# Kernel tuning notes

Measured on AMD Instinct MI355X. Metric: run time of the kernel, lower is better.

The kernel has to match this reference:

```python
import jax, jax.numpy as jnp
import numpy as np

B_SZ, L, D_MODEL = 2, 2048, 1024
EXPAND, N_STATE, K = 2, 16, 4
D_INNER = D_MODEL * EXPAND


def setup_inputs() -> dict:
    key = jax.random.key(0)
    ks = jax.random.split(key, 12)
    s = lambda k, shape, scale=0.02: jax.random.normal(k, shape, jnp.float32) * scale
    return {
        "x": jax.random.normal(ks[0], (B_SZ, L, D_MODEL), jnp.float32),
        "ln_gamma": jnp.ones((D_MODEL,), jnp.float32),
        "ln_beta": jnp.zeros((D_MODEL,), jnp.float32),
        "W_in": s(ks[1], (D_MODEL, 2 * D_INNER)),
        "conv_w": s(ks[2], (D_INNER, 1, K), 0.1),
        "conv_b": jnp.zeros((D_INNER,), jnp.float32),
        "A_log": jax.random.normal(ks[3], (N_STATE,), jnp.float32),
        "B_mat": s(ks[4], (N_STATE, D_INNER), 0.05),
        "C_mat": s(ks[5], (D_INNER, N_STATE), 0.05),
        "D_vec": s(ks[6], (D_INNER,), 0.1),
        "Wd": s(ks[7], (D_INNER, D_INNER)),
        "bd": jnp.zeros((D_INNER,), jnp.float32),
        "W_out": s(ks[8], (D_INNER, D_MODEL)),
    }


def _layernorm(x, g, b, eps=1e-5):
    mu = jnp.mean(x, axis=-1, keepdims=True)
    var = jnp.var(x, axis=-1, keepdims=True)
    return (x - mu) * jax.lax.rsqrt(var + eps) * g + b


def _selective_scan(x, delta, A, B_mat, C_mat, D_vec):
    # x: (b,l,d), delta: (b,l), A: (n,)
    dA = jnp.exp(delta[..., None] * A)            # (b,l,n)
    Bx = jnp.einsum('bld,nd->bln', x, B_mat) * delta[..., None]  # (b,l,n)

    def step(h, inp):
        dA_t, Bx_t = inp
        h = dA_t * h + Bx_t
        return h, h

    h0 = jnp.zeros((x.shape[0], A.shape[0]), x.dtype)
    # scan over seq axis
    _, hs = jax.lax.scan(step, h0, (jnp.swapaxes(dA, 0, 1), jnp.swapaxes(Bx, 0, 1)))
    hs = jnp.swapaxes(hs, 0, 1)                   # (b,l,n)
    return jnp.einsum('bln,dn->bld', hs, C_mat) + D_vec * x


def reference(x, ln_gamma, ln_beta, W_in, conv_w, conv_b, A_log, B_mat, C_mat, D_vec, Wd, bd, W_out):
    residual = x
    h = _layernorm(x, ln_gamma, ln_beta)
    xg = h @ W_in                                  # (b,l,2*d_inner)
    xs, gate = jnp.split(xg, 2, axis=-1)
    # depthwise causal conv (torch pads K-1 both sides then slices [:L] == left pad K-1)
    xc = jnp.swapaxes(xs, 1, 2)                    # (b,d,l)
    xc = jax.lax.conv_general_dilated(
        xc, conv_w, window_strides=(1,), padding=((K - 1, 0),),
        dimension_numbers=('NCH', 'OIH', 'NCH'), feature_group_count=D_INNER)
    xc = xc + conv_b[None, :, None]
    xs = jnp.swapaxes(xc, 1, 2)                    # (b,l,d)
    xs = jax.nn.silu(xs)
    # S4 kernel
    delta = jnp.mean(jax.nn.softplus(xs @ Wd + bd), axis=-1)  # (b,l)
    A = -jnp.exp(A_log)
    y = _selective_scan(xs, delta, A, B_mat, C_mat, D_vec)
    y = y * jax.nn.silu(gate)
    y = y @ W_out
    return residual + y
```

## Files before the change

kernel.cpp:

```cpp
#include <hip/hip_runtime.h>
#include <cstdint>
#include <cstddef>

typedef unsigned short u16;
typedef __attribute__((ext_vector_type(4))) float floatx4;
typedef __attribute__((ext_vector_type(8))) __bf16 bf16x8;

__device__ __forceinline__ float u2f(u16 u) {
    union { unsigned int i; float f; } x;
    x.i = ((unsigned int)u) << 16;
    return x.f;
}
__device__ __forceinline__ u16 f2u(float f) {
    union { float f; unsigned int i; } x;
    x.f = f;
    unsigned int r = x.i + 0x7fffu + ((x.i >> 16) & 1u);
    return (u16)(r >> 16);
}

__device__ __forceinline__ void swz(int bid, int& x, int& y) {
    int xcd = bid & 7;
    int lid = bid >> 3;
    x = lid >> 2;
    y = xcd * 4 + (lid & 3);
}

__device__ __forceinline__ void tr_tile(const float* __restrict__ in, u16* __restrict__ out,
                                        int K, int N, int bx, int by, float* tile ) {
    int n0 = bx * 32, k0 = by * 32;
    int tx = threadIdx.x & 31, ty = threadIdx.x >> 5;
#pragma unroll
    for (int j = 0; j < 4; ++j) {
        int r = ty + j * 8;
        tile[r * 33 + tx] = in[(size_t)(k0 + r) * N + n0 + tx];
    }
    __syncthreads();
#pragma unroll
    for (int j = 0; j < 4; ++j) {
        int r = ty + j * 8;
        out[(size_t)(n0 + r) * K + k0 + tx] = f2u(tile[tx * 33 + r]);
    }
}

__global__ __launch_bounds__(256)
void prep_kernel(const float* __restrict__ W_in, u16* __restrict__ Wt_in,
                 const float* __restrict__ Wd, u16* __restrict__ Wt_ext,
                 const float* __restrict__ W_out, u16* __restrict__ Wt_out,
                 const float* __restrict__ B_mat,
                 const float* __restrict__ x, const float* __restrict__ gamma,
                 const float* __restrict__ beta, u16* __restrict__ h,
                 float* __restrict__ out) {
    __shared__ float tile[32 * 33];
    int blk = blockIdx.x, t = threadIdx.x;
    if (blk < 4096) {
        tr_tile(W_in, Wt_in, 1024, 4096, blk & 127, blk >> 7, tile);
    } else if (blk < 8192) {
        int b2 = blk - 4096;
        tr_tile(Wd, Wt_ext, 2048, 2048, b2 & 63, b2 >> 6, tile);
    } else if (blk < 10240) {
        int b3 = blk - 8192;
        tr_tile(W_out, Wt_out, 2048, 1024, b3 & 31, b3 >> 5, tile);
    } else if (blk < 14336) {
        int r = blk - 10240;
        const float4* xr = (const float4*)(x + (size_t)r * 1024);
        float4 xv = xr[t];
        ((float4*)(out + (size_t)r * 1024))[t] = xv;
        float s = xv.x + xv.y + xv.z + xv.w;
        float ss = xv.x * xv.x + xv.y * xv.y + xv.z * xv.z + xv.w * xv.w;
#pragma unroll
        for (int off = 32; off > 0; off >>= 1) {
            s += __shfl_down(s, off, 64);
            ss += __shfl_down(ss, off, 64);
        }
        __shared__ float rs[4], rss[4], mu_s, ri_s;
        int wave = t >> 6, lane = t & 63;
        if (lane == 0) { rs[wave] = s; rss[wave] = ss; }
        __syncthreads();
        if (t == 0) {
            float S = rs[0] + rs[1] + rs[2] + rs[3];
            float SS = rss[0] + rss[1] + rss[2] + rss[3];
            float mu = S * (1.f / 1024.f);
            float var = SS * (1.f / 1024.f) - mu * mu;
            mu_s = mu;
            ri_s = rsqrtf(fmaxf(var, 0.f) + 1e-5f);
        }
        __syncthreads();
        float mu = mu_s, ri = ri_s;
        float4 gv = ((const float4*)gamma)[t];
        float4 bv = ((const float4*)beta)[t];
        ushort4 o;
        o.x = f2u((xv.x - mu) * ri * gv.x + bv.x);
        o.y = f2u((xv.y - mu) * ri * gv.y + bv.y);
        o.z = f2u((xv.z - mu) * ri * gv.z + bv.z);
        o.w = f2u((xv.w - mu) * ri * gv.w + bv.w);
        ((ushort4*)(h + (size_t)r * 1024))[t] = o;
    } else {
        int idx = (blk - 14336) * 256 + t;
        int row = 2048 + (idx >> 11), col = idx & 2047;
        u16 v = (row < 2064) ? f2u(B_mat[(size_t)(row - 2048) * 2048 + col]) : (u16)0;
        Wt_ext[(size_t)row * 2048 + col] = v;
    }
}

__device__ __forceinline__ void gl_lds16(const u16* g, u16* l) {
    __builtin_amdgcn_global_load_lds(
        (const __attribute__((address_space(1))) void*)g,
        (__attribute__((address_space(3))) void*)l, 16, 0, 0);
}

template <int EPI>
__device__ __forceinline__
void gemm128_body(const u16* __restrict__ A, const u16* __restrict__ Bt,
                  void* __restrict__ out, int M, int N, int K, int Ksub) {
    __shared__ u16 As[128 * 64];
    __shared__ u16 Bs[128 * 64];
    int bx, by;
    swz(blockIdx.x, bx, by);
    const int tid = threadIdx.x;
    const int wave = tid >> 6, lane = tid & 63;
    const int row0 = by * 128, col0 = bx * 128;
    const int koff = blockIdx.y * Ksub;
    const int l16 = lane & 15, q = lane >> 4;
    const int sRow = lane >> 2, sK = (lane & 3) * 8;

    floatx4 acc[4][4];
#pragma unroll
    for (int i = 0; i < 4; ++i)
#pragma unroll
        for (int j = 0; j < 4; ++j) acc[i][j] = (floatx4){0.f, 0.f, 0.f, 0.f};

    const u16* gA = A + (size_t)(row0 + wave * 32 + sRow) * K + koff + sK;
    const u16* gB = Bt + (size_t)(col0 + wave * 32 + sRow) * K + koff + sK;
    u16* lA = As + wave * 1024;
    u16* lB = Bs + wave * 1024;
    const int rowb = (wave >> 1) * 64, colb = (wave & 1) * 64;

    for (int k0 = 0; k0 < Ksub; k0 += 64) {
#pragma unroll
        for (int h = 0; h < 2; ++h) {
            gl_lds16(gA + h * 32, lA + h * 4096);
            gl_lds16(gA + (size_t)16 * K + h * 32, lA + h * 4096 + 512);
            gl_lds16(gB + h * 32, lB + h * 4096);
            gl_lds16(gB + (size_t)16 * K + h * 32, lB + h * 4096 + 512);
        }
        gA += 64; gB += 64;
        __syncthreads();
#pragma unroll
        for (int h = 0; h < 2; ++h) {
            bf16x8 af[4], bfr[4];
#pragma unroll
            for (int mi = 0; mi < 4; ++mi)
                af[mi] = *(const bf16x8*)(As + h * 4096 + (rowb + mi * 16 + l16) * 32 + q * 8);
#pragma unroll
            for (int ni = 0; ni < 4; ++ni)
                bfr[ni] = *(const bf16x8*)(Bs + h * 4096 + (colb + ni * 16 + l16) * 32 + q * 8);
#pragma unroll
            for (int mi = 0; mi < 4; ++mi)
#pragma unroll
                for (int ni = 0; ni < 4; ++ni)
                    acc[mi][ni] = __builtin_amdgcn_mfma_f32_16x16x32_bf16(
                        af[mi], bfr[ni], acc[mi][ni], 0, 0, 0);
        }
        __syncthreads();
    }

    const int mB = row0 + rowb;
    const int nB = col0 + colb + l16;
    if constexpr (EPI == 0) {
        u16* o = (u16*)out;
#pragma unroll
        for (int mi = 0; mi < 4; ++mi)
#pragma unroll
            for (int ni = 0; ni < 4; ++ni)
#pragma unroll
                for (int rr = 0; rr < 4; ++rr)
                    o[(size_t)(mB + mi * 16 + q * 4 + rr) * N + nB + ni * 16] =
                        f2u(acc[mi][ni][rr]);
    } else {
        float* C = (float*)out;
#pragma unroll
        for (int mi = 0; mi < 4; ++mi)
#pragma unroll
            for (int ni = 0; ni < 4; ++ni)
#pragma unroll
                for (int rr = 0; rr < 4; ++rr)
                    atomicAdd(&C[(size_t)(mB + mi * 16 + q * 4 + rr) * N + nB + ni * 16],
                              acc[mi][ni][rr]);
    }
}

__global__ __launch_bounds__(256)
void gemm_xg(const u16* __restrict__ A, const u16* __restrict__ Bt,
             u16* __restrict__ out, int M, int N, int K) {
    gemm128_body<0>(A, Bt, out, M, N, K, K);
}

__global__ __launch_bounds__(256)
void gemm_fin(const u16* __restrict__ A, const u16* __restrict__ Bt,
              void* __restrict__ out, int M, int N, int K, int Ksub) {
    gemm128_body<4>(A, Bt, out, M, N, K, Ksub);
}

__global__ __launch_bounds__(256)
void gemm_delta(const u16* __restrict__ A, const u16* __restrict__ Bt,
                float* __restrict__ dacc, const float* __restrict__ bias,
                float* __restrict__ Bdotn, int M, int N, int K) {
    __shared__ u16 As[128 * 128];
    __shared__ u16 Bs[64 * 128];
    int bx, by;
    swz(blockIdx.x, bx, by);
    const int tid = threadIdx.x;
    const int wave = tid >> 6, lane = tid & 63;
    const int row0 = by * 128, col0 = bx * 64;
    const int l16 = lane & 15, q = lane >> 4;
    const int sRow = lane >> 2, sK = (lane & 3) * 8;

    floatx4 acc[2][4];
#pragma unroll
    for (int i = 0; i < 2; ++i)
#pragma unroll
        for (int j = 0; j < 4; ++j) acc[i][j] = (floatx4){0.f, 0.f, 0.f, 0.f};

    const u16* gA = A + (size_t)(row0 + wave * 32 + sRow) * K + sK;
    const u16* gB = Bt + (size_t)(col0 + wave * 16 + sRow) * K + sK;
    u16* lA = As + wave * 1024;
    u16* lB = Bs + wave * 512;
    const int rowb = wave * 32;

    for (int k0 = 0; k0 < K; k0 += 128) {
#pragma unroll
        for (int h = 0; h < 4; ++h) {
            gl_lds16(gA + h * 32, lA + h * 4096);
            gl_lds16(gA + (size_t)16 * K + h * 32, lA + h * 4096 + 512);
            gl_lds16(gB + h * 32, lB + h * 2048);
        }
        gA += 128; gB += 128;
        __syncthreads();
#pragma unroll
        for (int h = 0; h < 4; ++h) {
            bf16x8 af[2], bfr[4];
#pragma unroll
            for (int mi = 0; mi < 2; ++mi)
                af[mi] = *(const bf16x8*)(As + h * 4096 + (rowb + mi * 16 + l16) * 32 + q * 8);
#pragma unroll
            for (int ni = 0; ni < 4; ++ni)
                bfr[ni] = *(const bf16x8*)(Bs + h * 2048 + (ni * 16 + l16) * 32 + q * 8);
#pragma unroll
            for (int mi = 0; mi < 2; ++mi)
#pragma unroll
                for (int ni = 0; ni < 4; ++ni)
                    acc[mi][ni] = __builtin_amdgcn_mfma_f32_16x16x32_bf16(
                        af[mi], bfr[ni], acc[mi][ni], 0, 0, 0);
        }
        __syncthreads();
    }

    const int mB = row0 + rowb;
    const int nB = col0 + l16;
    if (col0 < 2048) {
#pragma unroll
        for (int mi = 0; mi < 2; ++mi) {
#pragma unroll
            for (int rr = 0; rr < 4; ++rr) {
                float sv = 0.f;
#pragma unroll
                for (int ni = 0; ni < 4; ++ni) {
                    float t2 = acc[mi][ni][rr] + bias[nB + ni * 16];
                    sv += (t2 > 20.f) ? t2 : log1pf(expf(t2));
                }
#pragma unroll
                for (int off = 1; off < 16; off <<= 1)
                    sv += __shfl_xor(sv, off, 64);
                if (l16 == 0)
                    atomicAdd(&dacc[mB + mi * 16 + q * 4 + rr], sv);
            }
        }
    } else {
#pragma unroll
        for (int mi = 0; mi < 2; ++mi)
#pragma unroll
            for (int rr = 0; rr < 4; ++rr)
                Bdotn[(size_t)l16 * 4096 + mB + mi * 16 + q * 4 + rr] =
                    acc[mi][0][rr];
    }
}

__global__ __launch_bounds__(256) void conv_silu_kernel(const u16* __restrict__ xg,
                                                        const float* __restrict__ conv_w,
                                                        const float* __restrict__ conv_b,
                                                        u16* __restrict__ xsc,
                                                        float* __restrict__ delta_acc) {
    int r0 = blockIdx.x * 8;
    int l0 = r0 & 2047, bb = r0 >> 11;
    int t = threadIdx.x, d8 = t * 8;
    if (t < 8) delta_acc[r0 + t] = 0.f;

    ushort4 rw[11][2];
#pragma unroll
    for (int j = 0; j < 11; ++j) {
        int ls = l0 + j - 3;
        if (ls >= 0) {
            const u16* row = xg + (size_t)((bb << 11) + ls) * 4096 + d8;
            rw[j][0] = *(const ushort4*)row;
            rw[j][1] = *(const ushort4*)(row + 4);
        } else {
            rw[j][0] = (ushort4){0, 0, 0, 0};
            rw[j][1] = (ushort4){0, 0, 0, 0};
        }
    }
    float w[8][4];
#pragma unroll
    for (int j = 0; j < 8; ++j) {
        float4 wv = *(const float4*)(conv_w + (size_t)(d8 + j) * 4);
        w[j][0] = wv.x; w[j][1] = wv.y; w[j][2] = wv.z; w[j][3] = wv.w;
    }
    float cb[8];
    {
        float4 b0 = *(const float4*)(conv_b + d8);
        float4 b1 = *(const float4*)(conv_b + d8 + 4);
        cb[0] = b0.x; cb[1] = b0.y; cb[2] = b0.z; cb[3] = b0.w;
        cb[4] = b1.x; cb[5] = b1.y; cb[6] = b1.z; cb[7] = b1.w;
    }
#pragma unroll
    for (int i = 0; i < 8; ++i) {
        float xs[8];
#pragma unroll
        for (int j = 0; j < 8; ++j) xs[j] = cb[j];
#pragma unroll
        for (int k = 0; k < 4; ++k) {
            ushort4 u0 = rw[i + k][0], u1 = rw[i + k][1];
            xs[0] += w[0][k] * u2f(u0.x); xs[1] += w[1][k] * u2f(u0.y);
            xs[2] += w[2][k] * u2f(u0.z); xs[3] += w[3][k] * u2f(u0.w);
            xs[4] += w[4][k] * u2f(u1.x); xs[5] += w[5][k] * u2f(u1.y);
            xs[6] += w[6][k] * u2f(u1.z); xs[7] += w[7][k] * u2f(u1.w);
        }
        ushort4 o0, o1;
        o0.x = f2u(xs[0] / (1.f + expf(-xs[0])));
        o0.y = f2u(xs[1] / (1.f + expf(-xs[1])));
        o0.z = f2u(xs[2] / (1.f + expf(-xs[2])));
        o0.w = f2u(xs[3] / (1.f + expf(-xs[3])));
        o1.x = f2u(xs[4] / (1.f + expf(-xs[4])));
        o1.y = f2u(xs[5] / (1.f + expf(-xs[5])));
        o1.z = f2u(xs[6] / (1.f + expf(-xs[6])));
        o1.w = f2u(xs[7] / (1.f + expf(-xs[7])));
        u16* orow = xsc + (size_t)(r0 + i) * 2048 + d8;
        *(ushort4*)orow = o0;
        *(ushort4*)(orow + 4) = o1;
    }
}

__global__ __launch_bounds__(256) void scan_kernel(const float* __restrict__ delta_acc,
                                                   const float* __restrict__ Bdotn,
                                                   const float* __restrict__ A_log,
                                                   float* __restrict__ hsn) {
    int chain = blockIdx.x;
    int b = chain >> 4, n = chain & 15;
    int t = threadIdx.x;
    int wave = t >> 6, lane = t & 63;
    __shared__ float sd[2048], sb[2048];
    __shared__ float wA[4], wB[4];
#pragma unroll
    for (int m = 0; m < 2; ++m) {
        int idx = (m * 256 + t) * 4;
        *(float4*)(sd + idx) = *(const float4*)(delta_acc + b * 2048 + idx);
        *(float4*)(sb + idx) = *(const float4*)(Bdotn + (size_t)n * 4096 + b * 2048 + idx);
    }
    __syncthreads();
    float An = -expf(A_log[n]);
    int base = t * 8;
    float a[8], bb[8];
#pragma unroll
    for (int i = 0; i < 8; ++i) {
        float dl = sd[base + i] * (1.f / 2048.f);
        a[i] = expf(dl * An);
        bb[i] = sb[base + i] * dl;
    }
    float Aacc = 1.f, Bacc = 0.f;
#pragma unroll
    for (int i = 0; i < 8; ++i) {
        Bacc = a[i] * Bacc + bb[i];
        Aacc = a[i] * Aacc;
    }
#pragma unroll
    for (int d = 1; d < 64; d <<= 1) {
        float Ap = __shfl_up(Aacc, d, 64);
        float Bp = __shfl_up(Bacc, d, 64);
        if (lane >= d) {
            Bacc = Aacc * Bp + Bacc;
            Aacc = Aacc * Ap;
        }
    }
    if (lane == 63) { wA[wave] = Aacc; wB[wave] = Bacc; }
    float eA = __shfl_up(Aacc, 1, 64);
    float eB = __shfl_up(Bacc, 1, 64);
    if (lane == 0) { eA = 1.f; eB = 0.f; }
    __syncthreads();
    float pB = 0.f;
#pragma unroll
    for (int w = 0; w < 3; ++w)
        if (w < wave) pB = wA[w] * pB + wB[w];
    float h = eA * pB + eB;
#pragma unroll
    for (int i = 0; i < 8; ++i) {
        h = a[i] * h + bb[i];
        sd[base + i] = h;
    }
    __syncthreads();
#pragma unroll
    for (int m = 0; m < 2; ++m) {
        int idx = (m * 256 + t) * 4;
        *(float4*)(hsn + (size_t)n * 4096 + b * 2048 + idx) = *(const float4*)(sd + idx);
    }
}

__global__ __launch_bounds__(256) void ymid_kernel(const float* __restrict__ hsn,
                                                   const float* __restrict__ C_mat,
                                                   const float* __restrict__ D_vec,
                                                   const u16* __restrict__ xsc,
                                                   const u16* __restrict__ xg,
                                                   u16* __restrict__ ymid) {
    const int t = threadIdx.x;
    const int d0 = blockIdx.x * 512 + t * 2;
    const int r0 = blockIdx.y * 32;
    __shared__ float hsv[32 * 16];
#pragma unroll
    for (int k = 0; k < 2; ++k) {
        int idx = t * 2 + k;
        int rl = idx >> 4, nn = idx & 15;
        hsv[idx] = hsn[(size_t)nn * 4096 + r0 + rl];
    }
    float c0[16], c1[16];
#pragma unroll
    for (int k = 0; k < 4; ++k) {
        float4 v0 = *(const float4*)(C_mat + (size_t)d0 * 16 + k * 4);
        float4 v1 = *(const float4*)(C_mat + (size_t)(d0 + 1) * 16 + k * 4);
        c0[k * 4 + 0] = v0.x; c0[k * 4 + 1] = v0.y; c0[k * 4 + 2] = v0.z; c0[k * 4 + 3] = v0.w;
        c1[k * 4 + 0] = v1.x; c1[k * 4 + 1] = v1.y; c1[k * 4 + 2] = v1.z; c1[k * 4 + 3] = v1.w;
    }
    const float dv0 = D_vec[d0], dv1 = D_vec[d0 + 1];
    __syncthreads();
#pragma unroll 4
    for (int rl = 0; rl < 32; ++rl) {
        const int r = r0 + rl;
        float h0 = 0.f, h1 = 0.f;
#pragma unroll
        for (int nn = 0; nn < 16; ++nn) {
            float hv = hsv[rl * 16 + nn];
            h0 += hv * c0[nn];
            h1 += hv * c1[nn];
        }
        unsigned int xv = *(const unsigned int*)(xsc + (size_t)r * 2048 + d0);
        unsigned int gv = *(const unsigned int*)(xg + (size_t)r * 4096 + 2048 + d0);
        float x0 = u2f((u16)(xv & 0xffffu)), x1 = u2f((u16)(xv >> 16));
        float g0 = u2f((u16)(gv & 0xffffu)), g1 = u2f((u16)(gv >> 16));
        float y0 = (h0 + dv0 * x0) * (g0 / (1.f + expf(-g0)));
        float y1 = (h1 + dv1 * x1) * (g1 / (1.f + expf(-g1)));
        unsigned int o = (unsigned int)f2u(y0) | ((unsigned int)f2u(y1) << 16);
        *(unsigned int*)(ymid + (size_t)r * 2048 + d0) = o;
    }
}

extern "C" void kernel_launch(void* const* d_in, const int* in_sizes, int n_in,
                              void* d_out, int out_size, void* d_ws, size_t ws_size,
                              hipStream_t stream) {
    (void)in_sizes; (void)n_in;
    const float* x      = (const float*)d_in[0];
    const float* ln_g   = (const float*)d_in[1];
    const float* ln_b   = (const float*)d_in[2];
    const float* W_in   = (const float*)d_in[3];
    const float* conv_w = (const float*)d_in[4];
    const float* conv_b = (const float*)d_in[5];
    const float* A_log  = (const float*)d_in[6];
    const float* B_mat  = (const float*)d_in[7];
    const float* C_mat  = (const float*)d_in[8];
    const float* D_vec  = (const float*)d_in[9];
    const float* Wd     = (const float*)d_in[10];
    const float* bd     = (const float*)d_in[11];
    const float* W_out  = (const float*)d_in[12];
    float* out = (float*)d_out;

    char* base = (char*)d_ws;
    u16* Wt_in  = (u16*)base;
    u16* h_ln   = (u16*)base + 4096ull * 1024;
    u16* ymid   = (u16*)base;
    u16* Wt_ext = (u16*)(base + (16ull << 20));
    u16* Wt_out = (u16*)(base + (25ull << 20));
    u16* xg     = (u16*)(base + (29ull << 20));
    u16* xsc    = (u16*)(base + (61ull << 20));
    float* delta_acc = (float*)(base + (77ull << 20));
    float* Bdotn = delta_acc + 4096;
    float* hsn   = Bdotn + 16 * 4096;
    size_t needed = (77ull << 20) + 4096ull * 4 * (1 + 2 * 16);

    if (needed > ws_size) {
        hipMemsetAsync(d_out, 0x7F, (size_t)out_size * 4, stream);
        return;
    }

    prep_kernel<<<14848, 256, 0, stream>>>(W_in, Wt_in, Wd, Wt_ext, W_out, Wt_out,
                                           B_mat, x, ln_g, ln_b, h_ln, out);
    gemm_xg<<<1024, 256, 0, stream>>>(h_ln, Wt_in, xg, 4096, 4096, 1024);
    conv_silu_kernel<<<512, 256, 0, stream>>>(xg, conv_w, conv_b, xsc, delta_acc);
    gemm_delta<<<1056, 256, 0, stream>>>(xsc, Wt_ext, delta_acc, bd, Bdotn,
                                         4096, 2112, 2048);
    scan_kernel<<<32, 256, 0, stream>>>(delta_acc, Bdotn, A_log, hsn);
    ymid_kernel<<<dim3(4, 128), 256, 0, stream>>>(hsn, C_mat, D_vec, xsc, xg, ymid);
    gemm_fin<<<dim3(256, 2), 256, 0, stream>>>(ymid, Wt_out, out, 4096, 1024, 2048, 1024);
}
```

Measured before the change: 338.0 us.

## Split-K the delta GEMM into bf16 planes with a separate softplus reduction

```diff
diff --git a/kernel.cpp b/kernel.cpp
--- a/kernel.cpp
+++ b/kernel.cpp
@@ -202,6 +202,54 @@
 }
 
 __global__ __launch_bounds__(256)
+void gemm_delta_sk(const u16* __restrict__ A, const u16* __restrict__ Bt,
+                   u16* __restrict__ planes, int M, int N, int K, int Ksub) {
+    u16* plane = planes + (size_t)blockIdx.y * M * N;
+    gemm128_body<0>(A, Bt, plane, M, N, K, Ksub);
+}
+
+__global__ __launch_bounds__(256)
+void delta_reduce(const u16* __restrict__ planes, const float* __restrict__ bias,
+                  float* __restrict__ dacc, float* __restrict__ Bdotn) {
+    const int r = blockIdx.x;
+    const int t = threadIdx.x;
+    const size_t PL = (size_t)4096 * 2176;
+    const u16* p0 = planes + (size_t)r * 2176 + t * 8;
+    const u16* p1 = p0 + PL;
+    ushort4 a0 = *(const ushort4*)p0;
+    ushort4 a1 = *(const ushort4*)(p0 + 4);
+    ushort4 b0 = *(const ushort4*)p1;
+    ushort4 b1 = *(const ushort4*)(p1 + 4);
+    float4 c0 = *(const float4*)(bias + t * 8);
+    float4 c1 = *(const float4*)(bias + t * 8 + 4);
+    float e[8];
+    e[0] = u2f(a0.x) + u2f(b0.x) + c0.x;
+    e[1] = u2f(a0.y) + u2f(b0.y) + c0.y;
+    e[2] = u2f(a0.z) + u2f(b0.z) + c0.z;
+    e[3] = u2f(a0.w) + u2f(b0.w) + c0.w;
+    e[4] = u2f(a1.x) + u2f(b1.x) + c1.x;
+    e[5] = u2f(a1.y) + u2f(b1.y) + c1.y;
+    e[6] = u2f(a1.z) + u2f(b1.z) + c1.z;
+    e[7] = u2f(a1.w) + u2f(b1.w) + c1.w;
+    float sv = 0.f;
+#pragma unroll
+    for (int i = 0; i < 8; ++i)
+        sv += (e[i] > 20.f) ? e[i] : log1pf(expf(e[i]));
+#pragma unroll
+    for (int off = 32; off > 0; off >>= 1)
+        sv += __shfl_down(sv, off, 64);
+    __shared__ float wsum[4];
+    const int wave = t >> 6, lane = t & 63;
+    if (lane == 0) wsum[wave] = sv;
+    __syncthreads();
+    if (t == 0) dacc[r] = wsum[0] + wsum[1] + wsum[2] + wsum[3];
+    if (t < 16) {
+        const u16* q = planes + (size_t)r * 2176 + 2048 + t;
+        Bdotn[(size_t)t * 4096 + r] = u2f(*q) + u2f(*(q + PL));
+    }
+}
+
+__global__ __launch_bounds__(256)
 void gemm_delta(const u16* __restrict__ A, const u16* __restrict__ Bt,
                 float* __restrict__ dacc, const float* __restrict__ bias,
                 float* __restrict__ Bdotn, int M, int N, int K) {
@@ -490,19 +538,28 @@
     float* delta_acc = (float*)(base + (77ull << 20));
     float* Bdotn = delta_acc + 4096;
     float* hsn   = Bdotn + 16 * 4096;
+    u16* planes  = (u16*)(base + (78ull << 20));
     size_t needed = (77ull << 20) + 4096ull * 4 * (1 + 2 * 16);
+    size_t needed_sk = (78ull << 20) + 2ull * 4096 * 2176 * 2;
 
     if (needed > ws_size) {
         hipMemsetAsync(d_out, 0x7F, (size_t)out_size * 4, stream);
         return;
     }
+    const bool use_sk = (ws_size >= needed_sk);
 
     prep_kernel<<<14848, 256, 0, stream>>>(W_in, Wt_in, Wd, Wt_ext, W_out, Wt_out,
                                            B_mat, x, ln_g, ln_b, h_ln, out);
     gemm_xg<<<1024, 256, 0, stream>>>(h_ln, Wt_in, xg, 4096, 4096, 1024);
     conv_silu_kernel<<<512, 256, 0, stream>>>(xg, conv_w, conv_b, xsc, delta_acc);
-    gemm_delta<<<1056, 256, 0, stream>>>(xsc, Wt_ext, delta_acc, bd, Bdotn,
-                                         4096, 2112, 2048);
+    if (use_sk) {
+        gemm_delta_sk<<<dim3(544, 2), 256, 0, stream>>>(xsc, Wt_ext, planes,
+                                                        4096, 2176, 2048, 1024);
+        delta_reduce<<<4096, 256, 0, stream>>>(planes, bd, delta_acc, Bdotn);
+    } else {
+        gemm_delta<<<1056, 256, 0, stream>>>(xsc, Wt_ext, delta_acc, bd, Bdotn,
+                                             4096, 2112, 2048);
+    }
     scan_kernel<<<32, 256, 0, stream>>>(delta_acc, Bdotn, A_log, hsn);
     ymid_kernel<<<dim3(4, 128), 256, 0, stream>>>(hsn, C_mat, D_vec, xsc, xg, ymid);
     gemm_fin<<<dim3(256, 2), 256, 0, stream>>>(ymid, Wt_out, out, 4096, 1024, 2048, 1024);
```

After: 333.0 us. No clear change (-1.5%).
